# Kernel optimization log

Hardware: AMD Instinct MI355X
Metric: run time of the kernel (lower is better)

Reference implementation:

```python
import jax, jax.numpy as jnp
import numpy as np

HEADS = 8


def setup_inputs() -> dict:
    key = jax.random.key(0)
    ks = jax.random.split(key, 5)
    B, C, H, W = 2, 256, 48, 48
    s = 0.02
    return {
        "ct": jax.random.normal(ks[0], (B, C, H, W), jnp.float32),
        "us": jax.random.normal(ks[1], (B, C, H, W), jnp.float32),
        "w_qkv_ct": jax.random.normal(ks[2], (3 * C, C), jnp.float32) * s,
        "w_qkv_us": jax.random.normal(ks[3], (3 * C, C), jnp.float32) * s,
        "w_proj": jax.random.normal(ks[4], (C, 2 * C), jnp.float32) * s,
        "b_proj": jnp.zeros((C,), jnp.float32),
    }


def _heads_view(x, B, H, W):
    # [B, C, H, W] -> [B, heads, HW, dh]
    C = x.shape[1]
    return x.reshape(B, HEADS, C // HEADS, H * W).transpose(0, 1, 3, 2)


def _cross_attn(q, k, v, scale):
    # q,k,v: [B, heads, HW, dh]
    attn = jax.nn.softmax(jnp.einsum("bhnd,bhmd->bhnm", q, k) * scale, axis=-1)
    return jnp.einsum("bhnm,bhmd->bhnd", attn, v)


def reference(ct, us, w_qkv_ct, w_qkv_us, w_proj, b_proj):
    B, C, H, W = ct.shape
    dh = C // HEADS
    scale = dh ** (-0.5)

    # 1x1 convs as channel GEMMs
    qkv1 = jnp.einsum("oc,bchw->bohw", w_qkv_ct, ct)
    qkv2 = jnp.einsum("oc,bchw->bohw", w_qkv_us, us)
    q1, k1, v1 = jnp.split(qkv1, 3, axis=1)
    q2, k2, v2 = jnp.split(qkv2, 3, axis=1)

    # CT queries attend to US keys/values
    o1 = _cross_attn(_heads_view(q1, B, H, W), _heads_view(k2, B, H, W),
                     _heads_view(v2, B, H, W), scale)
    # US queries attend to CT keys/values
    o2 = _cross_attn(_heads_view(q2, B, H, W), _heads_view(k1, B, H, W),
                     _heads_view(v1, B, H, W), scale)

    # [B, heads, HW, dh] -> [B, C, H, W]
    out1 = o1.transpose(0, 1, 3, 2).reshape(B, C, H, W)
    out2 = o2.transpose(0, 1, 3, 2).reshape(B, C, H, W)

    fused = jnp.concatenate([ct + out1, us + out2], axis=1)
    return jnp.einsum("oc,bchw->bohw", w_proj, fused) + b_proj[None, :, None, None]
```

## Files before the change

kernel.cpp:

```cpp
#include <hip/hip_runtime.h>
#include <hip/hip_bf16.h>
#include <math.h>

#define HW   2304
#define CCH  256

#define QSCALE 0.25504368686637270f

typedef short short8 __attribute__((ext_vector_type(8)));
typedef float f32x4  __attribute__((ext_vector_type(4)));

__device__ inline unsigned short f2bf(float f) {
    union { float f; unsigned u; } v; v.f = f;
    unsigned r = v.u + 0x7FFF + ((v.u >> 16) & 1);
    return (unsigned short)(r >> 16);
}
__device__ inline unsigned pkbf2(float a, float b) {
    float2 f; f.x = a; f.y = b;
    union { __hip_bfloat162 h; unsigned u; } c;
    c.h = __float22bfloat162_rn(f);
    return c.u;
}
__device__ inline unsigned pktrunc(float a, float b) {
    return __builtin_amdgcn_perm(__builtin_bit_cast(unsigned, b),
                                 __builtin_bit_cast(unsigned, a), 0x07060302u);
}


__device__ __forceinline__ void prep_unit(
    int u, int t,
    const float* __restrict__ ct, const float* __restrict__ us,
    const float* __restrict__ w1, const float* __restrict__ w2,
    const float* __restrict__ w3,
    unsigned short* __restrict__ xT,
    unsigned short* __restrict__ wb1, unsigned short* __restrict__ wb2,
    unsigned short* __restrict__ w3b,
    unsigned short* __restrict__ Ts )
{
    if (u >= 576) {
        const int v_ = u - 576;
        int z, base;
        if (v_ < 192)      { z = 0; base = v_ * 1024; }
        else if (v_ < 384) { z = 1; base = (v_ - 192) * 1024; }
        else               { z = 2; base = (v_ - 384) * 1024; }
        const float* s = (z == 0) ? w1 : (z == 1) ? w2 : w3;
        unsigned short* d = (z == 0) ? wb1 : (z == 1) ? wb2 : w3b;
        const int i = base + t * 4;
        const float4 v4 = *(const float4*)&s[i];
        const float sc = (z < 2 && i < 65536) ? QSCALE : 1.f;
        uint2 p; p.x = pkbf2(v4.x * sc, v4.y * sc); p.y = pkbf2(v4.z * sc, v4.w * sc);
        *(uint2*)&d[i] = p;
        return;
    }
    const int pt = u % 36, rest = u / 36, ctile = rest & 3, z = rest >> 2;
    const float* __restrict__ src = ((z >> 1) ? us : ct) + (size_t)(z & 1) * CCH * HW;
    unsigned short* __restrict__ dst = xT + (size_t)z * HW * 256;
    const int p0 = pt * 64, c0 = ctile * 64;
    const int m = t & 15, ms = ((m >> 1) & 7) << 3;
    __syncthreads();
#pragma unroll
    for (int r = 0; r < 4; r++) {
        const int c = (t >> 4) + 16 * r;
        const float4 v4 = *(const float4*)&src[(size_t)(c0 + c) * HW + p0 + m * 4];
        const int cs = c ^ ms;
        Ts[(m * 4 + 0) * 72 + cs] = f2bf(v4.x);
        Ts[(m * 4 + 1) * 72 + cs] = f2bf(v4.y);
        Ts[(m * 4 + 2) * 72 + cs] = f2bf(v4.z);
        Ts[(m * 4 + 3) * 72 + cs] = f2bf(v4.w);
    }
    __syncthreads();
    const int p = t >> 2, c8 = (t & 3) * 16;
    const int es = ((p >> 3) & 7) << 3;
    const short8 a  = *(const short8*)&Ts[p * 72 + (c8 ^ es)];
    const short8 b8 = *(const short8*)&Ts[p * 72 + ((c8 + 8) ^ es)];
    *(short8*)&dst[(size_t)(p0 + p) * 256 + c0 + c8]     = a;
    *(short8*)&dst[(size_t)(p0 + p) * 256 + c0 + c8 + 8] = b8;
}

__device__ __forceinline__ void qkv_unit(
    int ptile, int otile, int z, int t,
    const unsigned short* __restrict__ xT,
    const unsigned short* __restrict__ wb1, const unsigned short* __restrict__ wb2,
    unsigned short* __restrict__ qkvT1, unsigned short* __restrict__ qkvT2,
    unsigned short* __restrict__ vdm1,  unsigned short* __restrict__ vdm2,
    unsigned short* __restrict__ Ws, unsigned short* __restrict__ Xs)
{
    const int inp = z >> 1, b = z & 1;
    const unsigned short* __restrict__ X = xT + (size_t)(inp * 2 + b) * HW * 256;
    const unsigned short* __restrict__ W = inp ? wb2 : wb1;
    unsigned short* __restrict__ qT = (inp ? qkvT2 : qkvT1) + (size_t)b * HW * 512;
    unsigned short* __restrict__ vd = (inp ? vdm2 : vdm1) + (size_t)b * CCH * HW;
    const int p0 = ptile * 64, o0 = otile * 64;
    const int w = t >> 6, lane = t & 63, quad = lane >> 4, m = lane & 15;
    const int sr = t >> 3, sc = t & 7;

    f32x4 acc[4] = {{0,0,0,0},{0,0,0,0},{0,0,0,0},{0,0,0,0}};

    short8 wv0 = *(const short8*)&W[(size_t)(o0 + sr) * 256 + sc * 8];
    short8 wv1 = *(const short8*)&W[(size_t)(o0 + 32 + sr) * 256 + sc * 8];
    short8 xv0 = *(const short8*)&X[(size_t)(p0 + sr) * 256 + sc * 8];
    short8 xv1 = *(const short8*)&X[(size_t)(p0 + 32 + sr) * 256 + sc * 8];

    for (int k0 = 0; k0 < 256; k0 += 64) {
        __syncthreads();
        *(short8*)&Ws[sr * 72 + sc * 8] = wv0;
        *(short8*)&Ws[(32 + sr) * 72 + sc * 8] = wv1;
        *(short8*)&Xs[sr * 72 + sc * 8] = xv0;
        *(short8*)&Xs[(32 + sr) * 72 + sc * 8] = xv1;
        __syncthreads();
        const int kn = k0 + 64;
        if (kn < 256) {
            wv0 = *(const short8*)&W[(size_t)(o0 + sr) * 256 + kn + sc * 8];
            wv1 = *(const short8*)&W[(size_t)(o0 + 32 + sr) * 256 + kn + sc * 8];
            xv0 = *(const short8*)&X[(size_t)(p0 + sr) * 256 + kn + sc * 8];
            xv1 = *(const short8*)&X[(size_t)(p0 + 32 + sr) * 256 + kn + sc * 8];
        }
#pragma unroll
        for (int kc2 = 0; kc2 < 2; kc2++) {
            const short8 af = *(const short8*)&Ws[(w * 16 + m) * 72 + kc2 * 32 + quad * 8];
#pragma unroll
            for (int pg = 0; pg < 4; pg++) {
                const short8 bf = *(const short8*)&Xs[(pg * 16 + m) * 72 + kc2 * 32 + quad * 8];
                acc[pg] = __builtin_amdgcn_mfma_f32_16x16x32_bf16(af, bf, acc[pg], 0, 0, 0);
            }
        }
    }
    __syncthreads();
    if (o0 < 512) {
#pragma unroll
        for (int pg = 0; pg < 4; pg++) {
            uint2 pk; pk.x = pkbf2(acc[pg][0], acc[pg][1]); pk.y = pkbf2(acc[pg][2], acc[pg][3]);
            *(uint2*)&Ws[(pg * 16 + m) * 72 + w * 16 + quad * 4] = pk;
        }
        __syncthreads();
        const int pr = t >> 2, cc = t & 3;
        const uint4 d0 = *(const uint4*)&Ws[pr * 72 + cc * 16];
        const uint4 d1 = *(const uint4*)&Ws[pr * 72 + cc * 16 + 8];
        *(uint4*)&qT[(size_t)(p0 + pr) * 512 + o0 + cc * 16]     = d0;
        *(uint4*)&qT[(size_t)(p0 + pr) * 512 + o0 + cc * 16 + 8] = d1;
    } else {
#pragma unroll
        for (int pg = 0; pg < 4; pg++)
#pragma unroll
            for (int r = 0; r < 4; r++)
                Ws[(w * 16 + quad * 4 + r) * 72 + pg * 16 + m] = f2bf(acc[pg][r]);
        __syncthreads();
        const int dr = t >> 2, cc = t & 3;
        const uint4 d0 = *(const uint4*)&Ws[dr * 72 + cc * 16];
        const uint4 d1 = *(const uint4*)&Ws[dr * 72 + cc * 16 + 8];
        *(uint4*)&vd[(size_t)(o0 - 512 + dr) * HW + p0 + cc * 16]     = d0;
        *(uint4*)&vd[(size_t)(o0 - 512 + dr) * HW + p0 + cc * 16 + 8] = d1;
    }
    __syncthreads();
}

__device__ __forceinline__ void proj_unit(
    int ptile, int otile, int t,
    const unsigned short* __restrict__ w3b, const unsigned short* __restrict__ fusedT,
    const float* __restrict__ bias, float* __restrict__ out,
    unsigned short* __restrict__ Ws, unsigned short* __restrict__ Xs)
{
    const int p0 = ptile * 64, o0 = otile * 64;
    const int w = t >> 6, lane = t & 63, quad = lane >> 4, m = lane & 15;
    const int sr = t >> 3, sc = t & 7;

    f32x4 acc[4] = {{0,0,0,0},{0,0,0,0},{0,0,0,0},{0,0,0,0}};

    short8 wv0 = *(const short8*)&w3b[(size_t)(o0 + sr) * 512 + sc * 8];
    short8 wv1 = *(const short8*)&w3b[(size_t)(o0 + 32 + sr) * 512 + sc * 8];
    short8 xv0 = *(const short8*)&fusedT[(size_t)(p0 + sr) * 512 + sc * 8];
    short8 xv1 = *(const short8*)&fusedT[(size_t)(p0 + 32 + sr) * 512 + sc * 8];

    for (int k0 = 0; k0 < 512; k0 += 64) {
        __syncthreads();
        *(short8*)&Ws[sr * 72 + sc * 8] = wv0;
        *(short8*)&Ws[(32 + sr) * 72 + sc * 8] = wv1;
        *(short8*)&Xs[sr * 72 + sc * 8] = xv0;
        *(short8*)&Xs[(32 + sr) * 72 + sc * 8] = xv1;
        __syncthreads();
        const int kn = k0 + 64;
        if (kn < 512) {
            wv0 = *(const short8*)&w3b[(size_t)(o0 + sr) * 512 + kn + sc * 8];
            wv1 = *(const short8*)&w3b[(size_t)(o0 + 32 + sr) * 512 + kn + sc * 8];
            xv0 = *(const short8*)&fusedT[(size_t)(p0 + sr) * 512 + kn + sc * 8];
            xv1 = *(const short8*)&fusedT[(size_t)(p0 + 32 + sr) * 512 + kn + sc * 8];
        }
#pragma unroll
        for (int kc2 = 0; kc2 < 2; kc2++) {
            const short8 af = *(const short8*)&Ws[(w * 16 + m) * 72 + kc2 * 32 + quad * 8];
#pragma unroll
            for (int pg = 0; pg < 4; pg++) {
                const short8 bf = *(const short8*)&Xs[(pg * 16 + m) * 72 + kc2 * 32 + quad * 8];
                acc[pg] = __builtin_amdgcn_mfma_f32_16x16x32_bf16(af, bf, acc[pg], 0, 0, 0);
            }
        }
    }
    const int b = (p0 >= HW) ? 1 : 0;
    const int pl0 = p0 - b * HW;
    float* __restrict__ ob = out + (size_t)b * CCH * HW;
    float b4[4];
#pragma unroll
    for (int r = 0; r < 4; r++) b4[r] = bias[o0 + w * 16 + quad * 4 + r];
#pragma unroll
    for (int pg = 0; pg < 4; pg++)
#pragma unroll
        for (int r = 0; r < 4; r++)
            ob[(size_t)(o0 + w * 16 + quad * 4 + r) * HW + pl0 + pg * 16 + m]
                = acc[pg][r] + b4[r];
}

__global__ __launch_bounds__(256, 4) void prep_k(
    const float* __restrict__ ct, const float* __restrict__ us,
    const float* __restrict__ w1, const float* __restrict__ w2,
    const float* __restrict__ w3,
    unsigned short* __restrict__ xT,
    unsigned short* __restrict__ b1, unsigned short* __restrict__ b2,
    unsigned short* __restrict__ b3)
{
    __shared__ __align__(16) unsigned short Ts[64 * 72];
    prep_unit(blockIdx.x, threadIdx.x, ct, us, w1, w2, w3, xT, b1, b2, b3, Ts);
}

__global__ __launch_bounds__(256, 4) void qkv_k(
    const unsigned short* __restrict__ xT,
    const unsigned short* __restrict__ wb1, const unsigned short* __restrict__ wb2,
    unsigned short* __restrict__ qkvT1, unsigned short* __restrict__ qkvT2,
    unsigned short* __restrict__ vdm1,  unsigned short* __restrict__ vdm2)
{
    __shared__ __align__(16) unsigned short Ws[64 * 72];
    __shared__ __align__(16) unsigned short Xs[64 * 72];
    qkv_unit(blockIdx.x, blockIdx.y, blockIdx.z, threadIdx.x,
             xT, wb1, wb2, qkvT1, qkvT2, vdm1, vdm2, Ws, Xs);
}

__global__ __launch_bounds__(256, 4) void attn_k(
    const unsigned short* __restrict__ qkvT1, const unsigned short* __restrict__ qkvT2,
    const unsigned short* __restrict__ vdm1,  const unsigned short* __restrict__ vdm2,
    const float* __restrict__ ct, const float* __restrict__ us,
    unsigned short* __restrict__ fusedT)
{
    __shared__ __align__(16) unsigned short Ks[2][128 * 32];
    __shared__ __align__(16) unsigned short Vs[2][32 * 136];
    const int t = threadIdx.x;

    const int ptile = blockIdx.x, dir = blockIdx.z;
    const int b = blockIdx.y >> 3, h = blockIdx.y & 7;

    const unsigned short* __restrict__ Qt = (dir ? qkvT2 : qkvT1) + (size_t)b * HW * 512;
    const unsigned short* __restrict__ Kt = (dir ? qkvT1 : qkvT2) + (size_t)b * HW * 512
                                            + 256 + h * 32;
    const unsigned short* __restrict__ Vd = (dir ? vdm1 : vdm2) + ((size_t)b * CCH + h * 32) * HW;
    const float* __restrict__ src = (dir ? us : ct) + ((size_t)b * CCH + h * 32) * HW;

    const int w = t >> 6, lane = t & 63, quad = lane >> 4, m = lane & 15;
    const int kj0 = t >> 2, kcs = t & 3;
    const int pcK = kcs ^ (((kj0 >> 1) & 1) | (((kj0 >> 3) & 1) << 1));
    const int vr0 = t >> 4, vcs = t & 15;
    const int g2m = ((m >> 1) & 1) | (((m >> 2) & 1) << 1);
    const int ksb_off = ((m >> 2) * 8 + (m & 3)) * 32 + (quad ^ g2m) * 8;
    const int vsb_off = m * 136 + quad * 8;
    const short ONE = (short)0x3F80;
    const short8 ones = {ONE,ONE,ONE,ONE,ONE,ONE,ONE,ONE};

    const int pqA = ptile * 128 + w * 32 + m;
    const short8 qfA = *(const short8*)&Qt[(size_t)pqA * 512 + h * 32 + quad * 8];
    const short8 qfB = *(const short8*)&Qt[(size_t)(pqA + 16) * 512 + h * 32 + quad * 8];

    f32x4 acc0A = {0,0,0,0}, acc1A = {0,0,0,0}, acclA = {0,0,0,0};
    f32x4 acc0B = {0,0,0,0}, acc1B = {0,0,0,0}, acclB = {0,0,0,0};

    short8 ka = *(const short8*)&Kt[(size_t)kj0 * 512 + kcs * 8];
    short8 kb = *(const short8*)&Kt[(size_t)(kj0 + 64) * 512 + kcs * 8];
    short8 va = *(const short8*)&Vd[(size_t)vr0 * HW + vcs * 8];
    short8 vb = *(const short8*)&Vd[(size_t)(vr0 + 16) * HW + vcs * 8];
    *(short8*)&Ks[0][kj0 * 32 + pcK * 8] = ka;
    *(short8*)&Ks[0][(kj0 + 64) * 32 + pcK * 8] = kb;
    *(short8*)&Vs[0][vr0 * 136 + vcs * 8] = va;
    *(short8*)&Vs[0][(vr0 + 16) * 136 + vcs * 8] = vb;
    ka = *(const short8*)&Kt[(size_t)(128 + kj0) * 512 + kcs * 8];
    kb = *(const short8*)&Kt[(size_t)(128 + kj0 + 64) * 512 + kcs * 8];
    va = *(const short8*)&Vd[(size_t)vr0 * HW + 128 + vcs * 8];
    vb = *(const short8*)&Vd[(size_t)(vr0 + 16) * HW + 128 + vcs * 8];
    __syncthreads();

    for (int ti = 0; ti < 18; ti++) {
        const int cur = ti & 1, nxt = cur ^ 1;
        if (ti < 17) {
            *(short8*)&Ks[nxt][kj0 * 32 + pcK * 8] = ka;
            *(short8*)&Ks[nxt][(kj0 + 64) * 32 + pcK * 8] = kb;
            *(short8*)&Vs[nxt][vr0 * 136 + vcs * 8] = va;
            *(short8*)&Vs[nxt][(vr0 + 16) * 136 + vcs * 8] = vb;
        }
        const int jn = (ti + 2) * 128;
        if (jn < HW) {
            ka = *(const short8*)&Kt[(size_t)(jn + kj0) * 512 + kcs * 8];
            kb = *(const short8*)&Kt[(size_t)(jn + kj0 + 64) * 512 + kcs * 8];
            va = *(const short8*)&Vd[(size_t)vr0 * HW + jn + vcs * 8];
            vb = *(const short8*)&Vd[(size_t)(vr0 + 16) * HW + jn + vcs * 8];
        }

        const unsigned short* __restrict__ ksb = &Ks[cur][ksb_off];
        const unsigned short* __restrict__ vsb = &Vs[cur][vsb_off];

        uint4 pwA[4], pwB[4];
#pragma unroll
        for (int f = 0; f < 8; f++) {
            const short8 kf = *(const short8*)(ksb + ((f >> 1) * 32 + (f & 1) * 4) * 32);
            const f32x4 z = {0,0,0,0};
            const f32x4 SA = __builtin_amdgcn_mfma_f32_16x16x32_bf16(kf, qfA, z, 0, 0, 0);
            const f32x4 SB = __builtin_amdgcn_mfma_f32_16x16x32_bf16(kf, qfB, z, 0, 0, 0);
            const float a0 = __builtin_amdgcn_exp2f(SA[0]);
            const float a1 = __builtin_amdgcn_exp2f(SA[1]);
            const float a2 = __builtin_amdgcn_exp2f(SA[2]);
            const float a3 = __builtin_amdgcn_exp2f(SA[3]);
            const float b0 = __builtin_amdgcn_exp2f(SB[0]);
            const float b1 = __builtin_amdgcn_exp2f(SB[1]);
            const float b2 = __builtin_amdgcn_exp2f(SB[2]);
            const float b3 = __builtin_amdgcn_exp2f(SB[3]);
            if ((f & 1) == 0) {
                pwA[f >> 1].x = pktrunc(a0, a1); pwA[f >> 1].y = pktrunc(a2, a3);
                pwB[f >> 1].x = pktrunc(b0, b1); pwB[f >> 1].y = pktrunc(b2, b3);
            } else {
                pwA[f >> 1].z = pktrunc(a0, a1); pwA[f >> 1].w = pktrunc(a2, a3);
                pwB[f >> 1].z = pktrunc(b0, b1); pwB[f >> 1].w = pktrunc(b2, b3);
            }
        }
#pragma unroll
        for (int kt = 0; kt < 4; kt++) {
            const short8 pfA = __builtin_bit_cast(short8, pwA[kt]);
            const short8 pfB = __builtin_bit_cast(short8, pwB[kt]);
            const short8 vf0 = *(const short8*)(vsb + kt * 32);
            const short8 vf1 = *(const short8*)(vsb + 16 * 136 + kt * 32);
            acc0A = __builtin_amdgcn_mfma_f32_16x16x32_bf16(vf0, pfA, acc0A, 0, 0, 0);
            acc1A = __builtin_amdgcn_mfma_f32_16x16x32_bf16(vf1, pfA, acc1A, 0, 0, 0);
            acclA = __builtin_amdgcn_mfma_f32_16x16x32_bf16(ones, pfA, acclA, 0, 0, 0);
            acc0B = __builtin_amdgcn_mfma_f32_16x16x32_bf16(vf0, pfB, acc0B, 0, 0, 0);
            acc1B = __builtin_amdgcn_mfma_f32_16x16x32_bf16(vf1, pfB, acc1B, 0, 0, 0);
            acclB = __builtin_amdgcn_mfma_f32_16x16x32_bf16(ones, pfB, acclB, 0, 0, 0);
        }
        __syncthreads();
    }

    const int cb = dir * 256 + h * 32, d0 = quad * 4;
    {
        const float inv = 1.f / acclA[0];
        unsigned short* __restrict__ fT = fusedT + ((size_t)b * HW + pqA) * 512 + cb + d0;
        uint2 s0, s1;
        s0.x = pkbf2(acc0A[0] * inv + src[(size_t)(d0 + 0) * HW + pqA],
                     acc0A[1] * inv + src[(size_t)(d0 + 1) * HW + pqA]);
        s0.y = pkbf2(acc0A[2] * inv + src[(size_t)(d0 + 2) * HW + pqA],
                     acc0A[3] * inv + src[(size_t)(d0 + 3) * HW + pqA]);
        s1.x = pkbf2(acc1A[0] * inv + src[(size_t)(16 + d0 + 0) * HW + pqA],
                     acc1A[1] * inv + src[(size_t)(16 + d0 + 1) * HW + pqA]);
        s1.y = pkbf2(acc1A[2] * inv + src[(size_t)(16 + d0 + 2) * HW + pqA],
                     acc1A[3] * inv + src[(size_t)(16 + d0 + 3) * HW + pqA]);
        *(uint2*)&fT[0]  = s0;
        *(uint2*)&fT[16] = s1;
    }
    {
        const int pqB = pqA + 16;
        const float inv = 1.f / acclB[0];
        unsigned short* __restrict__ fT = fusedT + ((size_t)b * HW + pqB) * 512 + cb + d0;
        uint2 s0, s1;
        s0.x = pkbf2(acc0B[0] * inv + src[(size_t)(d0 + 0) * HW + pqB],
                     acc0B[1] * inv + src[(size_t)(d0 + 1) * HW + pqB]);
        s0.y = pkbf2(acc0B[2] * inv + src[(size_t)(d0 + 2) * HW + pqB],
                     acc0B[3] * inv + src[(size_t)(d0 + 3) * HW + pqB]);
        s1.x = pkbf2(acc1B[0] * inv + src[(size_t)(16 + d0 + 0) * HW + pqB],
                     acc1B[1] * inv + src[(size_t)(16 + d0 + 1) * HW + pqB]);
        s1.y = pkbf2(acc1B[2] * inv + src[(size_t)(16 + d0 + 2) * HW + pqB],
                     acc1B[3] * inv + src[(size_t)(16 + d0 + 3) * HW + pqB]);
        *(uint2*)&fT[0]  = s0;
        *(uint2*)&fT[16] = s1;
    }
}

__global__ __launch_bounds__(256, 4) void proj_k(
    const unsigned short* __restrict__ w3b, const unsigned short* __restrict__ fusedT,
    const float* __restrict__ bias, float* __restrict__ out)
{
    __shared__ __align__(16) unsigned short Ws[64 * 72];
    __shared__ __align__(16) unsigned short Xs[64 * 72];
    proj_unit(blockIdx.x, blockIdx.y, threadIdx.x, w3b, fusedT, bias, out, Ws, Xs);
}

extern "C" void kernel_launch(void* const* d_in, const int* in_sizes, int n_in,
                              void* d_out, int out_size, void* d_ws, size_t ws_size,
                              hipStream_t stream)
{
    const float* ct       = (const float*)d_in[0];
    const float* us       = (const float*)d_in[1];
    const float* w_qkv_ct = (const float*)d_in[2];
    const float* w_qkv_us = (const float*)d_in[3];
    const float* w_proj   = (const float*)d_in[4];
    const float* b_proj   = (const float*)d_in[5];
    float* out = (float*)d_out;

    unsigned short* wb1   = (unsigned short*)d_ws;
    unsigned short* wb2   = wb1 + (size_t)768 * 256;
    unsigned short* w3b   = wb2 + (size_t)768 * 256;
    unsigned short* xT    = w3b + (size_t)256 * 512;
    unsigned short* qkvT1 = xT    + (size_t)4 * HW * 256;
    unsigned short* qkvT2 = qkvT1 + (size_t)2 * HW * 512;
    unsigned short* vdm1  = qkvT2 + (size_t)2 * HW * 512;
    unsigned short* vdm2  = vdm1  + (size_t)2 * CCH * HW;
    unsigned short* fusedT= vdm2  + (size_t)2 * CCH * HW;

    prep_k<<<dim3(1088), 256, 0, stream>>>(ct, us, w_qkv_ct, w_qkv_us, w_proj,
                                           xT, wb1, wb2, w3b);
    qkv_k <<<dim3(36, 12, 4), 256, 0, stream>>>(xT, wb1, wb2, qkvT1, qkvT2, vdm1, vdm2);
    attn_k<<<dim3(18, 16, 2), 256, 0, stream>>>(qkvT1, qkvT2, vdm1, vdm2, ct, us, fusedT);
    proj_k<<<dim3(72, 4), 256, 0, stream>>>(w3b, fusedT, b_proj, out);
}
```

Baseline: 128.9 us.

## Split attention over key dimension into two halves with separate combine kernel

Splits the attention key loop into two halves (split-K / flash-decoding style), doubling the attention grid from 576 to 1152 blocks. Each half writes unnormalized fp32 partial accumulators and row sums to workspace, and a new combine kernel sums them, normalizes, adds the residual and writes bf16 fusedT. This is meant to improve occupancy and CU utilization on the 256-CU device, at the cost of an extra kernel launch and extra fp32 partial traffic. Merging works without max rescaling because the softmax has no max subtraction.

```diff
diff --git a/kernel.cpp b/kernel.cpp
--- a/kernel.cpp
+++ b/kernel.cpp
@@ -236,21 +236,19 @@
 __global__ __launch_bounds__(256, 4) void attn_k(
     const unsigned short* __restrict__ qkvT1, const unsigned short* __restrict__ qkvT2,
     const unsigned short* __restrict__ vdm1,  const unsigned short* __restrict__ vdm2,
-    const float* __restrict__ ct, const float* __restrict__ us,
-    unsigned short* __restrict__ fusedT)
+    float* __restrict__ pacc, float* __restrict__ pl)
 {
     __shared__ __align__(16) unsigned short Ks[2][128 * 32];
     __shared__ __align__(16) unsigned short Vs[2][32 * 136];
     const int t = threadIdx.x;
 
     const int ptile = blockIdx.x, dir = blockIdx.z;
-    const int b = blockIdx.y >> 3, h = blockIdx.y & 7;
+    const int half = blockIdx.y >> 4, b = (blockIdx.y >> 3) & 1, h = blockIdx.y & 7;
 
     const unsigned short* __restrict__ Qt = (dir ? qkvT2 : qkvT1) + (size_t)b * HW * 512;
     const unsigned short* __restrict__ Kt = (dir ? qkvT1 : qkvT2) + (size_t)b * HW * 512
                                             + 256 + h * 32;
     const unsigned short* __restrict__ Vd = (dir ? vdm1 : vdm2) + ((size_t)b * CCH + h * 32) * HW;
-    const float* __restrict__ src = (dir ? us : ct) + ((size_t)b * CCH + h * 32) * HW;
 
     const int w = t >> 6, lane = t & 63, quad = lane >> 4, m = lane & 15;
     const int kj0 = t >> 2, kcs = t & 3;
@@ -262,6 +260,7 @@
     const short ONE = (short)0x3F80;
     const short8 ones = {ONE,ONE,ONE,ONE,ONE,ONE,ONE,ONE};
 
+    const int jb = half * 1152;
     const int pqA = ptile * 128 + w * 32 + m;
     const short8 qfA = *(const short8*)&Qt[(size_t)pqA * 512 + h * 32 + quad * 8];
     const short8 qfB = *(const short8*)&Qt[(size_t)(pqA + 16) * 512 + h * 32 + quad * 8];
@@ -269,30 +268,30 @@
     f32x4 acc0A = {0,0,0,0}, acc1A = {0,0,0,0}, acclA = {0,0,0,0};
     f32x4 acc0B = {0,0,0,0}, acc1B = {0,0,0,0}, acclB = {0,0,0,0};
 
-    short8 ka = *(const short8*)&Kt[(size_t)kj0 * 512 + kcs * 8];
-    short8 kb = *(const short8*)&Kt[(size_t)(kj0 + 64) * 512 + kcs * 8];
-    short8 va = *(const short8*)&Vd[(size_t)vr0 * HW + vcs * 8];
-    short8 vb = *(const short8*)&Vd[(size_t)(vr0 + 16) * HW + vcs * 8];
+    short8 ka = *(const short8*)&Kt[(size_t)(jb + kj0) * 512 + kcs * 8];
+    short8 kb = *(const short8*)&Kt[(size_t)(jb + kj0 + 64) * 512 + kcs * 8];
+    short8 va = *(const short8*)&Vd[(size_t)vr0 * HW + jb + vcs * 8];
+    short8 vb = *(const short8*)&Vd[(size_t)(vr0 + 16) * HW + jb + vcs * 8];
     *(short8*)&Ks[0][kj0 * 32 + pcK * 8] = ka;
     *(short8*)&Ks[0][(kj0 + 64) * 32 + pcK * 8] = kb;
     *(short8*)&Vs[0][vr0 * 136 + vcs * 8] = va;
     *(short8*)&Vs[0][(vr0 + 16) * 136 + vcs * 8] = vb;
-    ka = *(const short8*)&Kt[(size_t)(128 + kj0) * 512 + kcs * 8];
-    kb = *(const short8*)&Kt[(size_t)(128 + kj0 + 64) * 512 + kcs * 8];
-    va = *(const short8*)&Vd[(size_t)vr0 * HW + 128 + vcs * 8];
-    vb = *(const short8*)&Vd[(size_t)(vr0 + 16) * HW + 128 + vcs * 8];
+    ka = *(const short8*)&Kt[(size_t)(jb + 128 + kj0) * 512 + kcs * 8];
+    kb = *(const short8*)&Kt[(size_t)(jb + 128 + kj0 + 64) * 512 + kcs * 8];
+    va = *(const short8*)&Vd[(size_t)vr0 * HW + jb + 128 + vcs * 8];
+    vb = *(const short8*)&Vd[(size_t)(vr0 + 16) * HW + jb + 128 + vcs * 8];
     __syncthreads();
 
-    for (int ti = 0; ti < 18; ti++) {
+    for (int ti = 0; ti < 9; ti++) {
         const int cur = ti & 1, nxt = cur ^ 1;
-        if (ti < 17) {
+        if (ti < 8) {
             *(short8*)&Ks[nxt][kj0 * 32 + pcK * 8] = ka;
             *(short8*)&Ks[nxt][(kj0 + 64) * 32 + pcK * 8] = kb;
             *(short8*)&Vs[nxt][vr0 * 136 + vcs * 8] = va;
             *(short8*)&Vs[nxt][(vr0 + 16) * 136 + vcs * 8] = vb;
         }
-        const int jn = (ti + 2) * 128;
-        if (jn < HW) {
+        if (ti < 7) {
+            const int jn = jb + (ti + 2) * 128;
             ka = *(const short8*)&Kt[(size_t)(jn + kj0) * 512 + kcs * 8];
             kb = *(const short8*)&Kt[(size_t)(jn + kj0 + 64) * 512 + kcs * 8];
             va = *(const short8*)&Vd[(size_t)vr0 * HW + jn + vcs * 8];
@@ -341,38 +340,54 @@
         __syncthreads();
     }
 
-    const int cb = dir * 256 + h * 32, d0 = quad * 4;
+    const int qinst = (b * 2 + dir) * 8 + h;
+    const int d0 = quad * 4;
     {
-        const float inv = 1.f / acclA[0];
-        unsigned short* __restrict__ fT = fusedT + ((size_t)b * HW + pqA) * 512 + cb + d0;
-        uint2 s0, s1;
-        s0.x = pkbf2(acc0A[0] * inv + src[(size_t)(d0 + 0) * HW + pqA],
-                     acc0A[1] * inv + src[(size_t)(d0 + 1) * HW + pqA]);
-        s0.y = pkbf2(acc0A[2] * inv + src[(size_t)(d0 + 2) * HW + pqA],
-                     acc0A[3] * inv + src[(size_t)(d0 + 3) * HW + pqA]);
-        s1.x = pkbf2(acc1A[0] * inv + src[(size_t)(16 + d0 + 0) * HW + pqA],
-                     acc1A[1] * inv + src[(size_t)(16 + d0 + 1) * HW + pqA]);
-        s1.y = pkbf2(acc1A[2] * inv + src[(size_t)(16 + d0 + 2) * HW + pqA],
-                     acc1A[3] * inv + src[(size_t)(16 + d0 + 3) * HW + pqA]);
-        *(uint2*)&fT[0]  = s0;
-        *(uint2*)&fT[16] = s1;
-    }
-    {
-        const int pqB = pqA + 16;
-        const float inv = 1.f / acclB[0];
-        unsigned short* __restrict__ fT = fusedT + ((size_t)b * HW + pqB) * 512 + cb + d0;
-        uint2 s0, s1;
-        s0.x = pkbf2(acc0B[0] * inv + src[(size_t)(d0 + 0) * HW + pqB],
-                     acc0B[1] * inv + src[(size_t)(d0 + 1) * HW + pqB]);
-        s0.y = pkbf2(acc0B[2] * inv + src[(size_t)(d0 + 2) * HW + pqB],
-                     acc0B[3] * inv + src[(size_t)(d0 + 3) * HW + pqB]);
-        s1.x = pkbf2(acc1B[0] * inv + src[(size_t)(16 + d0 + 0) * HW + pqB],
-                     acc1B[1] * inv + src[(size_t)(16 + d0 + 1) * HW + pqB]);
-        s1.y = pkbf2(acc1B[2] * inv + src[(size_t)(16 + d0 + 2) * HW + pqB],
-                     acc1B[3] * inv + src[(size_t)(16 + d0 + 3) * HW + pqB]);
-        *(uint2*)&fT[0]  = s0;
-        *(uint2*)&fT[16] = s1;
-    }
+        float* __restrict__ pA = pacc + ((size_t)(half * 32 + qinst) * HW + pqA) * 32;
+        *(f32x4*)&pA[d0]      = acc0A;
+        *(f32x4*)&pA[16 + d0] = acc1A;
+        float* __restrict__ pB = pacc + ((size_t)(half * 32 + qinst) * HW + pqA + 16) * 32;
+        *(f32x4*)&pB[d0]      = acc0B;
+        *(f32x4*)&pB[16 + d0] = acc1B;
+    }
+    if (quad == 0) {
+        pl[(size_t)(half * 32 + qinst) * HW + pqA]      = acclA[0];
+        pl[(size_t)(half * 32 + qinst) * HW + pqA + 16] = acclB[0];
+    }
+}
+
+__global__ __launch_bounds__(256, 8) void comb_k(
+    const float* __restrict__ pacc, const float* __restrict__ pl,
+    const float* __restrict__ ct, const float* __restrict__ us,
+    unsigned short* __restrict__ fusedT)
+{
+    const int t = threadIdx.x;
+    const int ptile = blockIdx.x, dir = blockIdx.z;
+    const int b = blockIdx.y >> 3, h = blockIdx.y & 7;
+    const int qinst = (b * 2 + dir) * 8 + h;
+    const int pq = ptile * 64 + (t >> 2);
+    const int dseg = (t & 3) * 8;
+
+    const size_t i0 = ((size_t)qinst * HW + pq) * 32 + dseg;
+    const size_t i1 = ((size_t)(32 + qinst) * HW + pq) * 32 + dseg;
+    const f32x4 a0 = *(const f32x4*)&pacc[i0];
+    const f32x4 a1 = *(const f32x4*)&pacc[i0 + 4];
+    const f32x4 c0 = *(const f32x4*)&pacc[i1];
+    const f32x4 c1 = *(const f32x4*)&pacc[i1 + 4];
+    const float l = pl[(size_t)qinst * HW + pq] + pl[(size_t)(32 + qinst) * HW + pq];
+    const float inv = 1.f / l;
+
+    const float* __restrict__ src = (dir ? us : ct) + ((size_t)b * CCH + h * 32) * HW;
+    float e[8];
+#pragma unroll
+    for (int i = 0; i < 4; i++) e[i]     = (a0[i] + c0[i]) * inv + src[(size_t)(dseg + i) * HW + pq];
+#pragma unroll
+    for (int i = 0; i < 4; i++) e[4 + i] = (a1[i] + c1[i]) * inv + src[(size_t)(dseg + 4 + i) * HW + pq];
+
+    uint4 s;
+    s.x = pkbf2(e[0], e[1]); s.y = pkbf2(e[2], e[3]);
+    s.z = pkbf2(e[4], e[5]); s.w = pkbf2(e[6], e[7]);
+    *(uint4*)&fusedT[((size_t)b * HW + pq) * 512 + dir * 256 + h * 32 + dseg] = s;
 }
 
 __global__ __launch_bounds__(256, 4) void proj_k(
@@ -405,10 +420,13 @@
     unsigned short* vdm1  = qkvT2 + (size_t)2 * HW * 512;
     unsigned short* vdm2  = vdm1  + (size_t)2 * CCH * HW;
     unsigned short* fusedT= vdm2  + (size_t)2 * CCH * HW;
+    float* pacc = (float*)(fusedT + (size_t)2 * HW * 512);
+    float* pl   = pacc + (size_t)64 * HW * 32;
 
     prep_k<<<dim3(1088), 256, 0, stream>>>(ct, us, w_qkv_ct, w_qkv_us, w_proj,
                                            xT, wb1, wb2, w3b);
     qkv_k <<<dim3(36, 12, 4), 256, 0, stream>>>(xT, wb1, wb2, qkvT1, qkvT2, vdm1, vdm2);
-    attn_k<<<dim3(18, 16, 2), 256, 0, stream>>>(qkvT1, qkvT2, vdm1, vdm2, ct, us, fusedT);
+    attn_k<<<dim3(18, 32, 2), 256, 0, stream>>>(qkvT1, qkvT2, vdm1, vdm2, pacc, pl);
+    comb_k<<<dim3(36, 16, 2), 256, 0, stream>>>(pacc, pl, ct, us, fusedT);
     proj_k<<<dim3(72, 4), 256, 0, stream>>>(w3b, fusedT, b_proj, out);
 }
```

Result: no change. 127.4 us (-1.1%).

## Load K/V fragments directly from global into registers, dropping LDS staging

Applied to the files above, without the earlier changes.

The attention kernel no longer stages K and V tiles through double-buffered shared memory with __syncthreads. Each wave loads its K fragments straight from global memory one tile ahead, using register ping-pong, and loads its V fragments per step. This removes the LDS writes and reads and the block barriers. In exchange the four waves of a block each fetch the same K/V from global/L2 (a 4x redundancy), register pressure rises, and the occupancy hint drops from 4 to 3 blocks per CU.

```diff
diff --git a/kernel.cpp b/kernel.cpp
--- a/kernel.cpp
+++ b/kernel.cpp
@@ -233,16 +233,62 @@
              xT, wb1, wb2, qkvT1, qkvT2, vdm1, vdm2, Ws, Xs);
 }
 
-__global__ __launch_bounds__(256, 4) void attn_k(
+#define ATTN_STEP(J0, KFC, KFN)                                                   \
+  {                                                                               \
+    short8 vf0[4], vf1[4];                                                        \
+    _Pragma("unroll")                                                             \
+    for (int kt = 0; kt < 4; kt++) {                                              \
+        vf0[kt] = *(const short8*)&Vd[(size_t)m * HW + (J0) + kt * 32 + quad * 8];\
+        vf1[kt] = *(const short8*)&Vd[(size_t)(m + 16) * HW + (J0) + kt * 32 + quad * 8];\
+    }                                                                             \
+    const int jn_ = (J0) + 128;                                                   \
+    if (jn_ < HW) {                                                               \
+        _Pragma("unroll")                                                         \
+        for (int f = 0; f < 8; f++)                                               \
+            KFN[f] = *(const short8*)&Kt[(size_t)(jn_ + (f >> 1) * 32 + (f & 1) * 4 + rK) * 512 + quad * 8];\
+    }                                                                             \
+    uint4 pwA[4], pwB[4];                                                         \
+    _Pragma("unroll")                                                             \
+    for (int f = 0; f < 8; f++) {                                                 \
+        const f32x4 z = {0, 0, 0, 0};                                             \
+        const f32x4 SA = __builtin_amdgcn_mfma_f32_16x16x32_bf16(KFC[f], qfA, z, 0, 0, 0);\
+        const f32x4 SB = __builtin_amdgcn_mfma_f32_16x16x32_bf16(KFC[f], qfB, z, 0, 0, 0);\
+        const float a0 = __builtin_amdgcn_exp2f(SA[0]);                           \
+        const float a1 = __builtin_amdgcn_exp2f(SA[1]);                           \
+        const float a2 = __builtin_amdgcn_exp2f(SA[2]);                           \
+        const float a3 = __builtin_amdgcn_exp2f(SA[3]);                           \
+        const float b0 = __builtin_amdgcn_exp2f(SB[0]);                           \
+        const float b1 = __builtin_amdgcn_exp2f(SB[1]);                           \
+        const float b2 = __builtin_amdgcn_exp2f(SB[2]);                           \
+        const float b3 = __builtin_amdgcn_exp2f(SB[3]);                           \
+        if ((f & 1) == 0) {                                                       \
+            pwA[f >> 1].x = pktrunc(a0, a1); pwA[f >> 1].y = pktrunc(a2, a3);     \
+            pwB[f >> 1].x = pktrunc(b0, b1); pwB[f >> 1].y = pktrunc(b2, b3);     \
+        } else {                                                                  \
+            pwA[f >> 1].z = pktrunc(a0, a1); pwA[f >> 1].w = pktrunc(a2, a3);     \
+            pwB[f >> 1].z = pktrunc(b0, b1); pwB[f >> 1].w = pktrunc(b2, b3);     \
+        }                                                                         \
+    }                                                                             \
+    _Pragma("unroll")                                                             \
+    for (int kt = 0; kt < 4; kt++) {                                              \
+        const short8 pfA = __builtin_bit_cast(short8, pwA[kt]);                   \
+        const short8 pfB = __builtin_bit_cast(short8, pwB[kt]);                   \
+        acc0A = __builtin_amdgcn_mfma_f32_16x16x32_bf16(vf0[kt], pfA, acc0A, 0, 0, 0);\
+        acc1A = __builtin_amdgcn_mfma_f32_16x16x32_bf16(vf1[kt], pfA, acc1A, 0, 0, 0);\
+        acclA = __builtin_amdgcn_mfma_f32_16x16x32_bf16(ones, pfA, acclA, 0, 0, 0);\
+        acc0B = __builtin_amdgcn_mfma_f32_16x16x32_bf16(vf0[kt], pfB, acc0B, 0, 0, 0);\
+        acc1B = __builtin_amdgcn_mfma_f32_16x16x32_bf16(vf1[kt], pfB, acc1B, 0, 0, 0);\
+        acclB = __builtin_amdgcn_mfma_f32_16x16x32_bf16(ones, pfB, acclB, 0, 0, 0);\
+    }                                                                             \
+  }
+
+__global__ __launch_bounds__(256, 3) void attn_k(
     const unsigned short* __restrict__ qkvT1, const unsigned short* __restrict__ qkvT2,
     const unsigned short* __restrict__ vdm1,  const unsigned short* __restrict__ vdm2,
     const float* __restrict__ ct, const float* __restrict__ us,
     unsigned short* __restrict__ fusedT)
 {
-    __shared__ __align__(16) unsigned short Ks[2][128 * 32];
-    __shared__ __align__(16) unsigned short Vs[2][32 * 136];
     const int t = threadIdx.x;
-
     const int ptile = blockIdx.x, dir = blockIdx.z;
     const int b = blockIdx.y >> 3, h = blockIdx.y & 7;
 
@@ -253,12 +299,7 @@
     const float* __restrict__ src = (dir ? us : ct) + ((size_t)b * CCH + h * 32) * HW;
 
     const int w = t >> 6, lane = t & 63, quad = lane >> 4, m = lane & 15;
-    const int kj0 = t >> 2, kcs = t & 3;
-    const int pcK = kcs ^ (((kj0 >> 1) & 1) | (((kj0 >> 3) & 1) << 1));
-    const int vr0 = t >> 4, vcs = t & 15;
-    const int g2m = ((m >> 1) & 1) | (((m >> 2) & 1) << 1);
-    const int ksb_off = ((m >> 2) * 8 + (m & 3)) * 32 + (quad ^ g2m) * 8;
-    const int vsb_off = m * 136 + quad * 8;
+    const int rK = (m >> 2) * 8 + (m & 3);
     const short ONE = (short)0x3F80;
     const short8 ones = {ONE,ONE,ONE,ONE,ONE,ONE,ONE,ONE};
 
@@ -269,76 +310,14 @@
     f32x4 acc0A = {0,0,0,0}, acc1A = {0,0,0,0}, acclA = {0,0,0,0};
     f32x4 acc0B = {0,0,0,0}, acc1B = {0,0,0,0}, acclB = {0,0,0,0};
 
-    short8 ka = *(const short8*)&Kt[(size_t)kj0 * 512 + kcs * 8];
-    short8 kb = *(const short8*)&Kt[(size_t)(kj0 + 64) * 512 + kcs * 8];
-    short8 va = *(const short8*)&Vd[(size_t)vr0 * HW + vcs * 8];
-    short8 vb = *(const short8*)&Vd[(size_t)(vr0 + 16) * HW + vcs * 8];
-    *(short8*)&Ks[0][kj0 * 32 + pcK * 8] = ka;
-    *(short8*)&Ks[0][(kj0 + 64) * 32 + pcK * 8] = kb;
-    *(short8*)&Vs[0][vr0 * 136 + vcs * 8] = va;
-    *(short8*)&Vs[0][(vr0 + 16) * 136 + vcs * 8] = vb;
-    ka = *(const short8*)&Kt[(size_t)(128 + kj0) * 512 + kcs * 8];
-    kb = *(const short8*)&Kt[(size_t)(128 + kj0 + 64) * 512 + kcs * 8];
-    va = *(const short8*)&Vd[(size_t)vr0 * HW + 128 + vcs * 8];
-    vb = *(const short8*)&Vd[(size_t)(vr0 + 16) * HW + 128 + vcs * 8];
-    __syncthreads();
-
-    for (int ti = 0; ti < 18; ti++) {
-        const int cur = ti & 1, nxt = cur ^ 1;
-        if (ti < 17) {
-            *(short8*)&Ks[nxt][kj0 * 32 + pcK * 8] = ka;
-            *(short8*)&Ks[nxt][(kj0 + 64) * 32 + pcK * 8] = kb;
-            *(short8*)&Vs[nxt][vr0 * 136 + vcs * 8] = va;
-            *(short8*)&Vs[nxt][(vr0 + 16) * 136 + vcs * 8] = vb;
-        }
-        const int jn = (ti + 2) * 128;
-        if (jn < HW) {
-            ka = *(const short8*)&Kt[(size_t)(jn + kj0) * 512 + kcs * 8];
-            kb = *(const short8*)&Kt[(size_t)(jn + kj0 + 64) * 512 + kcs * 8];
-            va = *(const short8*)&Vd[(size_t)vr0 * HW + jn + vcs * 8];
-            vb = *(const short8*)&Vd[(size_t)(vr0 + 16) * HW + jn + vcs * 8];
-        }
-
-        const unsigned short* __restrict__ ksb = &Ks[cur][ksb_off];
-        const unsigned short* __restrict__ vsb = &Vs[cur][vsb_off];
-
-        uint4 pwA[4], pwB[4];
-#pragma unroll
-        for (int f = 0; f < 8; f++) {
-            const short8 kf = *(const short8*)(ksb + ((f >> 1) * 32 + (f & 1) * 4) * 32);
-            const f32x4 z = {0,0,0,0};
-            const f32x4 SA = __builtin_amdgcn_mfma_f32_16x16x32_bf16(kf, qfA, z, 0, 0, 0);
-            const f32x4 SB = __builtin_amdgcn_mfma_f32_16x16x32_bf16(kf, qfB, z, 0, 0, 0);
-            const float a0 = __builtin_amdgcn_exp2f(SA[0]);
-            const float a1 = __builtin_amdgcn_exp2f(SA[1]);
-            const float a2 = __builtin_amdgcn_exp2f(SA[2]);
-            const float a3 = __builtin_amdgcn_exp2f(SA[3]);
-            const float b0 = __builtin_amdgcn_exp2f(SB[0]);
-            const float b1 = __builtin_amdgcn_exp2f(SB[1]);
-            const float b2 = __builtin_amdgcn_exp2f(SB[2]);
-            const float b3 = __builtin_amdgcn_exp2f(SB[3]);
-            if ((f & 1) == 0) {
-                pwA[f >> 1].x = pktrunc(a0, a1); pwA[f >> 1].y = pktrunc(a2, a3);
-                pwB[f >> 1].x = pktrunc(b0, b1); pwB[f >> 1].y = pktrunc(b2, b3);
-            } else {
-                pwA[f >> 1].z = pktrunc(a0, a1); pwA[f >> 1].w = pktrunc(a2, a3);
-                pwB[f >> 1].z = pktrunc(b0, b1); pwB[f >> 1].w = pktrunc(b2, b3);
-            }
-        }
-#pragma unroll
-        for (int kt = 0; kt < 4; kt++) {
-            const short8 pfA = __builtin_bit_cast(short8, pwA[kt]);
-            const short8 pfB = __builtin_bit_cast(short8, pwB[kt]);
-            const short8 vf0 = *(const short8*)(vsb + kt * 32);
-            const short8 vf1 = *(const short8*)(vsb + 16 * 136 + kt * 32);
-            acc0A = __builtin_amdgcn_mfma_f32_16x16x32_bf16(vf0, pfA, acc0A, 0, 0, 0);
-            acc1A = __builtin_amdgcn_mfma_f32_16x16x32_bf16(vf1, pfA, acc1A, 0, 0, 0);
-            acclA = __builtin_amdgcn_mfma_f32_16x16x32_bf16(ones, pfA, acclA, 0, 0, 0);
-            acc0B = __builtin_amdgcn_mfma_f32_16x16x32_bf16(vf0, pfB, acc0B, 0, 0, 0);
-            acc1B = __builtin_amdgcn_mfma_f32_16x16x32_bf16(vf1, pfB, acc1B, 0, 0, 0);
-            acclB = __builtin_amdgcn_mfma_f32_16x16x32_bf16(ones, pfB, acclB, 0, 0, 0);
-        }
-        __syncthreads();
+    short8 kf0[8], kf1[8];
+#pragma unroll
+    for (int f = 0; f < 8; f++)
+        kf0[f] = *(const short8*)&Kt[(size_t)((f >> 1) * 32 + (f & 1) * 4 + rK) * 512 + quad * 8];
+
+    for (int j0 = 0; j0 < HW; j0 += 256) {
+        ATTN_STEP(j0,       kf0, kf1);
+        ATTN_STEP(j0 + 128, kf1, kf0);
     }
 
     const int cb = dir * 256 + h * 32, d0 = quad * 4;
```

After: 198.1 us. 53.7% more time.
